# Optimization experiments

Hardware: AMD Instinct MI355X
Metric: run time of the kernel (lower is better)

The kernel has to match this reference:

```python
import jax, jax.numpy as jnp
import numpy as np

N_HEADS = 8  # head_dim = 640 / 8 = 80


def _split_heads(x):
    # [B, S, D] -> [B, H, S, D/H]
    B, S, D = x.shape
    return x.reshape(B, S, N_HEADS, D // N_HEADS).transpose(0, 2, 1, 3)


def _merge_heads(x):
    # [B, H, S, d] -> [B, S, H*d]
    B, H, S, d = x.shape
    return x.transpose(0, 2, 1, 3).reshape(B, S, H * d)


def setup_inputs() -> dict:
    key = jax.random.key(0)
    ks = jax.random.split(key, 12)
    B, S, D, C, A = 4, 2048, 640, 768, 16

    def w(k, fan_in, fan_out, s=1.0):
        return (jax.random.normal(k, (fan_in, fan_out), jnp.float32) / np.sqrt(fan_in) * s)

    return {
        "hidden_states": jax.random.normal(ks[0], (B, S, D), jnp.float32),
        "au_embedding": jax.random.normal(ks[1], (B, A, C), jnp.float32),
        "w_q": w(ks[2], D, D),
        "w_k": w(ks[3], D, D),
        "w_v": w(ks[4], D, D),
        "w_ak": w(ks[5], C, D),
        "w_av": w(ks[6], C, D),
        "w_g1": w(ks[7], D, D // 2),
        "b_g1": jnp.zeros((D // 2,), jnp.float32),
        "w_g2": w(ks[8], D // 2, D, s=0.02),  # near-zero per nn.init.zeros_
        "b_g2": jnp.full((D,), -1.5, jnp.float32),  # per nn.init.constant_(-1.5)
        "w_out": w(ks[9], D, D),
        "b_out": jnp.zeros((D,), jnp.float32),
        "temperature": jnp.full((1,), 5.0, jnp.float32),
    }


def reference(hidden_states, au_embedding, w_q, w_k, w_v, w_ak, w_av,
              w_g1, b_g1, w_g2, b_g2, w_out, b_out, temperature):
    au_scale = 1.0
    residual = hidden_states

    q = _split_heads(hidden_states @ w_q)  # [B,H,S,d]
    k = _split_heads(hidden_states @ w_k)
    v = _split_heads(hidden_states @ w_v)
    d = q.shape[-1]
    scale = 1.0 / jnp.sqrt(jnp.asarray(d, q.dtype))  # attn.scale = head_dim**-0.5

    # main self-attention: QK^T * scale -> softmax -> PV
    probs = jax.nn.softmax(jnp.einsum('bhqd,bhkd->bhqk', q, k) * scale, axis=-1)
    hs = _merge_heads(jnp.einsum('bhqk,bhkd->bhqd', probs, v))  # [B,S,D]

    # AU cross-attention with temperature-scaled logits
    au_k = _split_heads(au_embedding @ w_ak)  # [B,H,A,d]
    au_v = _split_heads(au_embedding @ w_av)
    scaled_alpha = scale * temperature[0]
    au_probs = jax.nn.softmax(jnp.einsum('bhqd,bhkd->bhqk', q, au_k) * scaled_alpha, axis=-1)
    au_hs = _merge_heads(jnp.einsum('bhqk,bhkd->bhqd', au_probs, au_v))  # [B,S,D]

    # gated MLP fusion: sigmoid(Linear(SiLU(Linear(au_hs))))
    gate = jax.nn.sigmoid(jax.nn.silu(au_hs @ w_g1 + b_g1) @ w_g2 + b_g2)
    hs = hs + au_scale * (gate * au_hs)

    hs = hs @ w_out + b_out  # to_out[0]; to_out[1] dropout is identity in eval
    return hs + residual  # residual_connection=True, rescale_output_factor=1.0
```

## Files before the change

### kernel.cpp

```cpp
#include <hip/hip_runtime.h>
#include <stdint.h>

typedef __attribute__((ext_vector_type(8))) short short8;
typedef __attribute__((ext_vector_type(4))) short short4v;
typedef __attribute__((ext_vector_type(4))) float f32x4;

#define DEV static __device__ __forceinline__

DEV short f2bf(float f) {
  union { float f; uint32_t u; } v; v.f = f;
  uint32_t r = (v.u + 0x7fffu + ((v.u >> 16) & 1u)) >> 16;
  return (short)(uint16_t)r;
}
DEV float bf2f(short s) {
  union { uint32_t u; float f; } v; v.u = ((uint32_t)(uint16_t)s) << 16;
  return v.f;
}
DEV int imin(int a, int b) { return a < b ? a : b; }
DEV int xcd_swz(int bid, int nwg) {
  int q8 = nwg >> 3, r8 = nwg & 7;
  int xcd = bid & 7, lin = bid >> 3;
  return (xcd < r8 ? xcd * (q8 + 1) : r8 * (q8 + 1) + (xcd - r8) * q8) + lin;
}


__global__ void k_detect(const uint32_t* __restrict__ src, int* __restrict__ flag) {
  __shared__ int cnt;
  if (threadIdx.x == 0) cnt = 0;
  __syncthreads();
  uint32_t u = src[threadIdx.x];
  int e = (int)((u >> 7) & 0xffu);
  if (e >= 110 && e <= 135) atomicAdd(&cnt, 1);
  __syncthreads();
  if (threadIdx.x == 0) *flag = (cnt > 128) ? 1 : 0;
}

__global__ void k_conv_vec(const void* __restrict__ s1, short* __restrict__ d1, int n1,
                           const void* __restrict__ s2, short* __restrict__ d2, int n2,
                           const int* __restrict__ flag) {
  int i = blockIdx.x * 256 + threadIdx.x;
  const void* src; short* dst;
  if (i < n1) { src = s1; dst = d1; }
  else if (i < n1 + n2) { src = s2; dst = d2; i -= n1; }
  else return;
  if (*flag) {
    ((short4v*)dst)[i] = ((const short4v*)src)[i];
  } else {
    f32x4 v = ((const f32x4*)src)[i];
    short4v o;
    o[0] = f2bf(v[0]); o[1] = f2bf(v[1]); o[2] = f2bf(v[2]); o[3] = f2bf(v[3]);
    ((short4v*)dst)[i] = o;
  }
}

struct WDesc { const void* src; short* dst; int K, N, dstride, tile0; };
struct WTable { WDesc d[8]; };

__global__ void k_conv_w(WTable tb, const int* __restrict__ flag) {
  __shared__ float tile[32][33];
  int tid = blockIdx.x;
  int idx = 0;
#pragma unroll
  for (int i = 1; i < 8; i++) if (tid >= tb.d[i].tile0) idx = i;
  WDesc wd = tb.d[idx];
  int local = tid - wd.tile0;
  int ntiles = wd.N >> 5;
  int n0 = (local % ntiles) * 32, k0 = (local / ntiles) * 32;
  int tx = threadIdx.x, ty = threadIdx.y;
  int isbf = *flag;
#pragma unroll
  for (int i = 0; i < 4; i++) {
    int r = k0 + ty + i * 8, c = n0 + tx;
    float v = 0.f;
    if (r < wd.K && c < wd.N)
      v = isbf ? bf2f(((const short*)wd.src)[(size_t)r * wd.N + c])
               : ((const float*)wd.src)[(size_t)r * wd.N + c];
    tile[ty + i * 8][tx] = v;
  }
  __syncthreads();
#pragma unroll
  for (int i = 0; i < 4; i++) {
    int n = n0 + ty + i * 8, k = k0 + tx;
    if (n < wd.N && k < wd.K) wd.dst[(size_t)n * wd.dstride + k] = f2bf(tile[tx][ty + i * 8]);
  }
}

__global__ void k_conv_bias(const void* b1, const void* b2, const void* b3, const void* tp,
                            float* B1, float* B2, float* B3, float* T,
                            const int* __restrict__ flag) {
  int i = blockIdx.x * 256 + threadIdx.x;
  int isbf = *flag;
  const void* s; float* d; int j;
  if (i < 320) { s = b1; d = B1; j = i; }
  else if (i < 960) { s = b2; d = B2; j = i - 320; }
  else if (i < 1600) { s = b3; d = B3; j = i - 960; }
  else if (i == 1600) { s = tp; d = T; j = 0; }
  else return;
  d[j] = isbf ? bf2f(((const short*)s)[j]) : ((const float*)s)[j];
}

template <int EPI>
__global__ __launch_bounds__(256) void k_gemm_bt(
    const short* __restrict__ A, const short* __restrict__ Wt, void* __restrict__ Cout,
    int M, int N, int K, int nbx,
    const float* __restrict__ bias, const short* __restrict__ x1,
    const short* __restrict__ x2, const short* __restrict__ res) {
  __shared__ __align__(16) short As[128 * 64];
  __shared__ __align__(16) short Bs[128 * 64];
  const int t = threadIdx.x;
  const int w = t >> 6, ln = t & 63;
  const int wm = w >> 1, wn = w & 1;
  const int swz = xcd_swz(blockIdx.x, gridDim.x);
  const int m0 = (swz / nbx) * 128, n0 = (swz % nbx) * 128;
  const int lrow = ln & 15, lg = ln >> 4;

  f32x4 acc[4][4];
#pragma unroll
  for (int i = 0; i < 4; i++)
#pragma unroll
    for (int j = 0; j < 4; j++) acc[i][j] = (f32x4){0.f, 0.f, 0.f, 0.f};

  for (int k0 = 0; k0 < K; k0 += 64) {
    __syncthreads();
#pragma unroll
    for (int c = 0; c < 4; c++) {
      int cc = c * 256 + t;
      int r = cc >> 3, col = (cc & 7) * 8;
      int ra = imin(m0 + r, M - 1);
      int rb = imin(n0 + r, N - 1);
      __builtin_amdgcn_global_load_lds(
          (const __attribute__((address_space(1))) void*)(A + (size_t)ra * K + k0 + col),
          (__attribute__((address_space(3))) void*)&As[(c * 256 + w * 64) * 8],
          16, 0, 0);
      __builtin_amdgcn_global_load_lds(
          (const __attribute__((address_space(1))) void*)(Wt + (size_t)rb * K + k0 + col),
          (__attribute__((address_space(3))) void*)&Bs[(c * 256 + w * 64) * 8],
          16, 0, 0);
    }
    __syncthreads();
    short8 af[4][2], bfr[4][2];
#pragma unroll
    for (int i = 0; i < 4; i++)
#pragma unroll
      for (int kk = 0; kk < 2; kk++) {
        af[i][kk] = *(const short8*)&As[(wm * 64 + i * 16 + lrow) * 64 + lg * 8 + kk * 32];
        bfr[i][kk] = *(const short8*)&Bs[(wn * 64 + i * 16 + lrow) * 64 + lg * 8 + kk * 32];
      }
    __builtin_amdgcn_s_setprio(1);
#pragma unroll
    for (int kk = 0; kk < 2; kk++)
#pragma unroll
      for (int i = 0; i < 4; i++)
#pragma unroll
        for (int j = 0; j < 4; j++)
          acc[i][j] = __builtin_amdgcn_mfma_f32_16x16x32_bf16(af[i][kk], bfr[j][kk], acc[i][j], 0, 0, 0);
    __builtin_amdgcn_s_setprio(0);
  }

  const int rb0 = m0 + wm * 64 + lg * 4;
#pragma unroll
  for (int i = 0; i < 4; i++) {
#pragma unroll
    for (int j = 0; j < 4; j++) {
      int col = n0 + wn * 64 + j * 16 + lrow;
      if (col >= N) continue;
#pragma unroll
      for (int r = 0; r < 4; r++) {
        int row = rb0 + i * 16 + r;
        if (row >= M) continue;
        float v = acc[i][j][r];
        size_t off = (size_t)row * N + col;
        if (EPI == 0) {
          ((short*)Cout)[off] = f2bf(v);
        } else if (EPI == 1) {
          float x = v + bias[col];
          ((short*)Cout)[off] = f2bf(x / (1.f + __expf(-x)));
        } else if (EPI == 2) {
          float g = 1.f / (1.f + __expf(-(v + bias[col])));
          ((short*)Cout)[off] = f2bf(bf2f(x1[off]) + g * bf2f(x2[off]));
        } else {
          ((float*)Cout)[off] = v + bias[col] + bf2f(res[off]);
        }
      }
    }
  }
}

__global__ __launch_bounds__(256) void k_build_vt(const short* __restrict__ qkv,
                                                  short* __restrict__ vt) {
  __shared__ __align__(16) short T[128 * 80];
  const int bh = blockIdx.y, st = blockIdx.x;
  const int b = bh >> 3, h = bh & 7;
  const int t = threadIdx.x;
  for (int c = t; c < 1280; c += 256) {
    int r = c / 10, blk = c % 10;
    *(short8*)&T[r * 80 + blk * 8] =
        *(const short8*)(qkv + (size_t)(b * 2048 + st * 128 + r) * 1920 + 1280 + h * 80 + blk * 8);
  }
  __syncthreads();
  for (int c = t; c < 1280; c += 256) {
    int dd = c % 80, qc = (c / 80) * 8;
    short8 v;
#pragma unroll
    for (int i = 0; i < 8; i++) {
      int q = qc + i;
      int tile = q >> 6, p = q & 63;
      int src = (tile << 6) + (p >> 2) + ((p & 3) << 4);
      v[i] = T[src * 80 + dd];
    }
    *(short8*)(vt + ((size_t)bh * 80 + dd) * 2048 + st * 128 + qc) = v;
  }
}

__global__ __launch_bounds__(512) void k_attn(const short* __restrict__ qkv,
                                              const short* __restrict__ vt,
                                              short* __restrict__ outp) {
  __shared__ __align__(16) short Ks[64 * 104];
  __shared__ __align__(16) char Vs[80 * 128];
  __shared__ __align__(16) char Ps[8][2048];

  const int swzb = xcd_swz(blockIdx.x, 512);
  const int qt = swzb & 15, bh = swzb >> 4;
  const int b = bh >> 3, h = bh & 7;
  const int t = threadIdx.x, w = t >> 6, ln = t & 63;
  const int lg = ln >> 4, lr = ln & 15;
  const float sc2 = 0.111803398875f * 1.4426950408889634f;
  const float SHIFT2 = 32.0f;

  short8 qfrag[3];
  {
    const short* qrow = qkv + (size_t)(b * 2048 + qt * 128 + w * 16 + lr) * 1920 + h * 80;
#pragma unroll
    for (int ks = 0; ks < 3; ks++) {
      int off = ks * 32 + lg * 8;
      short8 v = {0, 0, 0, 0, 0, 0, 0, 0};
      if (off < 80) v = *(const short8*)(qrow + off);
      qfrag[ks] = v;
    }
  }

  const short* kbase = qkv + (size_t)b * 2048 * 1920 + 640 + h * 80;
  const short* vbase = vt + (size_t)bh * 80 * 2048;

  int kr0 = t / 12, kb0 = t % 12;
  int kr1 = (t + 512) / 12, kb1 = (t + 512) % 12;
  int vr0 = t >> 3, vb0 = t & 7;
  int vr1 = (t + 512) >> 3, vb1 = (t + 512) & 7;
  const bool kv1 = (t < 256), vv1 = (t < 128);

  short8 kreg0 = {0,0,0,0,0,0,0,0}, kreg1 = kreg0, vreg0 = kreg0, vreg1 = kreg0;

  if (kb0 < 10) kreg0 = *(const short8*)(kbase + (size_t)kr0 * 1920 + kb0 * 8);
  if (kv1 && kb1 < 10) kreg1 = *(const short8*)(kbase + (size_t)kr1 * 1920 + kb1 * 8);
  vreg0 = *(const short8*)(vbase + (size_t)vr0 * 2048 + vb0 * 8);
  if (vv1) vreg1 = *(const short8*)(vbase + (size_t)vr1 * 2048 + vb1 * 8);

  f32x4 oacc[5];
#pragma unroll
  for (int f = 0; f < 5; f++) oacc[f] = (f32x4){0.f, 0.f, 0.f, 0.f};
  float psacc[4] = {0.f, 0.f, 0.f, 0.f};

  for (int kt = 0; kt < 32; kt++) {
    __syncthreads();
    *(short8*)&Ks[kr0 * 104 + kb0 * 8] = kreg0;
    if (kv1) *(short8*)&Ks[kr1 * 104 + kb1 * 8] = kreg1;
    {
      int dst0 = (vr0 * 128 + vb0 * 16) ^ ((vr0 & 7) << 4);
      *(short8*)&Vs[dst0] = vreg0;
      if (vv1) {
        int dst1 = (vr1 * 128 + vb1 * 16) ^ ((vr1 & 7) << 4);
        *(short8*)&Vs[dst1] = vreg1;
      }
    }
    __syncthreads();

    if (kt < 31) {
      const short* kb2 = kbase + (size_t)(kt + 1) * 64 * 1920;
      const short* vb2 = vbase + (size_t)(kt + 1) * 64;
      if (kb0 < 10) kreg0 = *(const short8*)(kb2 + (size_t)kr0 * 1920 + kb0 * 8);
      if (kv1 && kb1 < 10) kreg1 = *(const short8*)(kb2 + (size_t)kr1 * 1920 + kb1 * 8);
      vreg0 = *(const short8*)(vb2 + (size_t)vr0 * 2048 + vb0 * 8);
      if (vv1) vreg1 = *(const short8*)(vb2 + (size_t)vr1 * 2048 + vb1 * 8);
    }

    f32x4 sf[4];
#pragma unroll
    for (int j = 0; j < 4; j++) sf[j] = (f32x4){0.f, 0.f, 0.f, 0.f};
    __builtin_amdgcn_s_setprio(1);
#pragma unroll
    for (int ks = 0; ks < 3; ks++) {
#pragma unroll
      for (int j = 0; j < 4; j++) {
        short8 bk = *(const short8*)&Ks[(j * 16 + lr) * 104 + ks * 32 + lg * 8];
        sf[j] = __builtin_amdgcn_mfma_f32_16x16x32_bf16(qfrag[ks], bk, sf[j], 0, 0, 0);
      }
    }
    __builtin_amdgcn_s_setprio(0);

    char* Pw = Ps[w];
#pragma unroll
    for (int r = 0; r < 4; r++) {
      int row = lg * 4 + r;
      float p0 = exp2f(sf[0][r] * sc2 - SHIFT2);
      float p1 = exp2f(sf[1][r] * sc2 - SHIFT2);
      float p2 = exp2f(sf[2][r] * sc2 - SHIFT2);
      float p3 = exp2f(sf[3][r] * sc2 - SHIFT2);
      psacc[r] += (p0 + p1) + (p2 + p3);
      short4v pk;
      pk[0] = f2bf(p0); pk[1] = f2bf(p1); pk[2] = f2bf(p2); pk[3] = f2bf(p3);
      int addr = (row * 128 + lr * 8) ^ ((row & 7) << 4);
      *(short4v*)&Pw[addr] = pk;
    }

    __builtin_amdgcn_s_setprio(1);
#pragma unroll
    for (int ks = 0; ks < 2; ks++) {
      short8 ap = *(const short8*)&Pw[(lr * 128 + ks * 64 + lg * 16) ^ ((lr & 7) << 4)];
#pragma unroll
      for (int f = 0; f < 5; f++) {
        int vrow = f * 16 + lr;
        short8 bv = *(const short8*)&Vs[(vrow * 128 + ks * 64 + lg * 16) ^ ((vrow & 7) << 4)];
        oacc[f] = __builtin_amdgcn_mfma_f32_16x16x32_bf16(ap, bv, oacc[f], 0, 0, 0);
      }
    }
    __builtin_amdgcn_s_setprio(0);
  }

  float lrowv[4];
#pragma unroll
  for (int r = 0; r < 4; r++) {
    float sum = psacc[r];
#pragma unroll
    for (int off = 8; off >= 1; off >>= 1) sum += __shfl_xor(sum, off, 64);
    lrowv[r] = sum;
  }

#pragma unroll
  for (int f = 0; f < 5; f++) {
#pragma unroll
    for (int r = 0; r < 4; r++) {
      int q = qt * 128 + w * 16 + lg * 4 + r;
      float o = oacc[f][r] / lrowv[r];
      outp[(size_t)(b * 2048 + q) * 640 + h * 80 + f * 16 + lr] = f2bf(o);
    }
  }
}

__global__ __launch_bounds__(256) void k_au_attn(const short* __restrict__ qkv,
                                                 const short* __restrict__ aukv,
                                                 const float* __restrict__ temp,
                                                 short* __restrict__ auhs) {
  __shared__ __align__(16) short aK[16 * 640];
  __shared__ __align__(16) short aV[16 * 640];
  const int b = blockIdx.y;
  const int t = threadIdx.x;
  for (int c = t; c < 2560; c += 256) {
    int arr = c / 1280, cc = c - arr * 1280;
    int r = cc / 80, blk = cc % 80;
    const short* s = aukv + (size_t)(b * 16 + r) * 1280 + arr * 640 + blk * 8;
    short* d = (arr ? aV : aK) + r * 640 + blk * 8;
    *(short8*)d = *(const short8*)s;
  }
  __syncthreads();
  const int sl = t & 31, h = t >> 5;
  const int s = blockIdx.x * 32 + sl;
  const float alpha = 0.111803398875f * temp[0];
  const float LOG2E = 1.4426950408889634f;

  float qf[80];
  {
    const short* q = qkv + (size_t)(b * 2048 + s) * 1920 + h * 80;
#pragma unroll
    for (int c = 0; c < 10; c++) {
      short8 v = *(const short8*)(q + c * 8);
#pragma unroll
      for (int j = 0; j < 8; j++) qf[c * 8 + j] = bf2f(v[j]);
    }
  }
  float lgt[16];
#pragma unroll
  for (int a = 0; a < 16; a++) {
    const short* kr = &aK[a * 640 + h * 80];
    float acc = 0.f;
#pragma unroll
    for (int c = 0; c < 10; c++) {
      short8 v = *(const short8*)(kr + c * 8);
#pragma unroll
      for (int j = 0; j < 8; j++) acc += qf[c * 8 + j] * bf2f(v[j]);
    }
    lgt[a] = acc * alpha;
  }
  float m = lgt[0];
#pragma unroll
  for (int a = 1; a < 16; a++) m = fmaxf(m, lgt[a]);
  float se = 0.f;
#pragma unroll
  for (int a = 0; a < 16; a++) { lgt[a] = exp2f((lgt[a] - m) * LOG2E); se += lgt[a]; }
  float inv = 1.f / se;

  float o[80];
#pragma unroll
  for (int i = 0; i < 80; i++) o[i] = 0.f;
#pragma unroll
  for (int a = 0; a < 16; a++) {
    float pa = lgt[a] * inv;
    const short* vr = &aV[a * 640 + h * 80];
#pragma unroll
    for (int c = 0; c < 10; c++) {
      short8 v = *(const short8*)(vr + c * 8);
#pragma unroll
      for (int j = 0; j < 8; j++) o[c * 8 + j] += pa * bf2f(v[j]);
    }
  }
  short* op = auhs + (size_t)(b * 2048 + s) * 640 + h * 80;
#pragma unroll
  for (int c = 0; c < 10; c++) {
    short8 v;
#pragma unroll
    for (int j = 0; j < 8; j++) v[j] = f2bf(o[c * 8 + j]);
    *(short8*)(op + c * 8) = v;
  }
}

extern "C" void kernel_launch(void* const* d_in, const int* in_sizes, int n_in,
                              void* d_out, int out_size, void* d_ws, size_t ws_size,
                              hipStream_t stream) {
  (void)in_sizes; (void)n_in; (void)out_size; (void)ws_size;

  const void* hidden = d_in[0];
  const void* auemb  = d_in[1];

  char* ws = (char*)d_ws;
  int* FLAG   = (int*)(ws + 0);
  float* BG1  = (float*)(ws + 1024);
  float* BG2  = (float*)(ws + 4096);
  float* BOUT = (float*)(ws + 8192);
  float* TEMP = (float*)(ws + 12288);

  size_t o = 16384;
  short* HSB = (short*)(ws + o);    o += 10485760;
  short* AUB = (short*)(ws + o);    o += 98304;
  short* WQKVT = (short*)(ws + o);  o += 2457600;
  short* WAKVT = (short*)(ws + o);  o += 1966080;
  short* WG1T = (short*)(ws + o);   o += 409600;
  short* WG2T = (short*)(ws + o);   o += 409600;
  short* WOUTT = (short*)(ws + o);  o += 819200;
  short* QKV = (short*)(ws + o);    o += 31457280;
  short* VT = (short*)(ws + o);     o += 10485760;
  short* AUKV = (short*)(ws + o);   o += 163840;
  short* HSATTN = (short*)(ws + o); o += 10485760;
  short* AUHS = (short*)(ws + o);   o += 10485760;
  short* G1 = QKV;
  short* HSMIX = QKV + 5242880;

  k_detect<<<1, 256, 0, stream>>>((const uint32_t*)hidden, FLAG);

  k_conv_vec<<<5168, 256, 0, stream>>>(hidden, HSB, 1310720, auemb, AUB, 12288, FLAG);

  WTable tb;
  tb.d[0] = { d_in[2],  WQKVT,              640, 640, 640, 0    };
  tb.d[1] = { d_in[3],  WQKVT + 409600,     640, 640, 640, 400  };
  tb.d[2] = { d_in[4],  WQKVT + 819200,     640, 640, 640, 800  };
  tb.d[3] = { d_in[5],  WAKVT,              768, 640, 768, 1200 };
  tb.d[4] = { d_in[6],  WAKVT + 640 * 768,  768, 640, 768, 1680 };
  tb.d[5] = { d_in[7],  WG1T,               640, 320, 640, 2160 };
  tb.d[6] = { d_in[9],  WG2T,               320, 640, 320, 2360 };
  tb.d[7] = { d_in[11], WOUTT,              640, 640, 640, 2560 };
  k_conv_w<<<2960, dim3(32, 8), 0, stream>>>(tb, FLAG);
  k_conv_bias<<<7, 256, 0, stream>>>(d_in[8], d_in[10], d_in[12], d_in[13],
                                     BG1, BG2, BOUT, TEMP, FLAG);

  k_gemm_bt<0><<<960, 256, 0, stream>>>(HSB, WQKVT, QKV, 8192, 1920, 640, 15,
                                        nullptr, nullptr, nullptr, nullptr);
  k_gemm_bt<0><<<10, 256, 0, stream>>>(AUB, WAKVT, AUKV, 64, 1280, 768, 10,
                                       nullptr, nullptr, nullptr, nullptr);

  k_build_vt<<<dim3(16, 32), 256, 0, stream>>>(QKV, VT);
  k_attn<<<512, 512, 0, stream>>>(QKV, VT, HSATTN);
  k_au_attn<<<dim3(64, 4), 256, 0, stream>>>(QKV, AUKV, TEMP, AUHS);

  k_gemm_bt<1><<<192, 256, 0, stream>>>(AUHS, WG1T, G1, 8192, 320, 640, 3,
                                        BG1, nullptr, nullptr, nullptr);
  k_gemm_bt<2><<<320, 256, 0, stream>>>(G1, WG2T, HSMIX, 8192, 640, 320, 5,
                                        BG2, HSATTN, AUHS, nullptr);
  k_gemm_bt<3><<<320, 256, 0, stream>>>(HSMIX, WOUTT, d_out, 8192, 640, 640, 5,
                                        BOUT, nullptr, nullptr, HSB);
}
```

Measured before the change: 344.6 us.

## Merge prep, projection, and AU-attention launches into fewer fused kernels

```diff
diff --git a/kernel.cpp b/kernel.cpp
--- a/kernel.cpp
+++ b/kernel.cpp
@@ -4,6 +4,7 @@
 typedef __attribute__((ext_vector_type(8))) short short8;
 typedef __attribute__((ext_vector_type(4))) short short4v;
 typedef __attribute__((ext_vector_type(4))) float f32x4;
+typedef __attribute__((ext_vector_type(2))) uint32_t u32x2;
 
 #define DEV static __device__ __forceinline__
 
@@ -16,102 +17,98 @@
   union { uint32_t u; float f; } v; v.u = ((uint32_t)(uint16_t)s) << 16;
   return v.f;
 }
+DEV uint32_t fbits(float f) { union { float f; uint32_t u; } v; v.f = f; return v.u; }
 DEV int imin(int a, int b) { return a < b ? a : b; }
 DEV int xcd_swz(int bid, int nwg) {
   int q8 = nwg >> 3, r8 = nwg & 7;
   int xcd = bid & 7, lin = bid >> 3;
   return (xcd < r8 ? xcd * (q8 + 1) : r8 * (q8 + 1) + (xcd - r8) * q8) + lin;
 }
-
-
-__global__ void k_detect(const uint32_t* __restrict__ src, int* __restrict__ flag) {
+DEV int detect_flag(const uint32_t* src, int t) {
   __shared__ int cnt;
-  if (threadIdx.x == 0) cnt = 0;
+  if (t == 0) cnt = 0;
   __syncthreads();
-  uint32_t u = src[threadIdx.x];
+  uint32_t u = src[t & 255];
   int e = (int)((u >> 7) & 0xffu);
   if (e >= 110 && e <= 135) atomicAdd(&cnt, 1);
   __syncthreads();
-  if (threadIdx.x == 0) *flag = (cnt > 128) ? 1 : 0;
-}
-
-__global__ void k_conv_vec(const void* __restrict__ s1, short* __restrict__ d1, int n1,
-                           const void* __restrict__ s2, short* __restrict__ d2, int n2,
-                           const int* __restrict__ flag) {
-  int i = blockIdx.x * 256 + threadIdx.x;
-  const void* src; short* dst;
-  if (i < n1) { src = s1; dst = d1; }
-  else if (i < n1 + n2) { src = s2; dst = d2; i -= n1; }
-  else return;
-  if (*flag) {
-    ((short4v*)dst)[i] = ((const short4v*)src)[i];
-  } else {
-    f32x4 v = ((const f32x4*)src)[i];
-    short4v o;
-    o[0] = f2bf(v[0]); o[1] = f2bf(v[1]); o[2] = f2bf(v[2]); o[3] = f2bf(v[3]);
-    ((short4v*)dst)[i] = o;
-  }
-}
+  return cnt > 128;
+}
+
 
 struct WDesc { const void* src; short* dst; int K, N, dstride, tile0; };
 struct WTable { WDesc d[8]; };
 
-__global__ void k_conv_w(WTable tb, const int* __restrict__ flag) {
-  __shared__ float tile[32][33];
-  int tid = blockIdx.x;
-  int idx = 0;
-#pragma unroll
-  for (int i = 1; i < 8; i++) if (tid >= tb.d[i].tile0) idx = i;
-  WDesc wd = tb.d[idx];
-  int local = tid - wd.tile0;
-  int ntiles = wd.N >> 5;
-  int n0 = (local % ntiles) * 32, k0 = (local / ntiles) * 32;
-  int tx = threadIdx.x, ty = threadIdx.y;
-  int isbf = *flag;
-#pragma unroll
-  for (int i = 0; i < 4; i++) {
-    int r = k0 + ty + i * 8, c = n0 + tx;
-    float v = 0.f;
-    if (r < wd.K && c < wd.N)
-      v = isbf ? bf2f(((const short*)wd.src)[(size_t)r * wd.N + c])
-               : ((const float*)wd.src)[(size_t)r * wd.N + c];
-    tile[ty + i * 8][tx] = v;
-  }
-  __syncthreads();
-#pragma unroll
-  for (int i = 0; i < 4; i++) {
-    int n = n0 + ty + i * 8, k = k0 + tx;
-    if (n < wd.N && k < wd.K) wd.dst[(size_t)n * wd.dstride + k] = f2bf(tile[tx][ty + i * 8]);
-  }
-}
-
-__global__ void k_conv_bias(const void* b1, const void* b2, const void* b3, const void* tp,
-                            float* B1, float* B2, float* B3, float* T,
-                            const int* __restrict__ flag) {
-  int i = blockIdx.x * 256 + threadIdx.x;
-  int isbf = *flag;
-  const void* s; float* d; int j;
-  if (i < 320) { s = b1; d = B1; j = i; }
-  else if (i < 960) { s = b2; d = B2; j = i - 320; }
-  else if (i < 1600) { s = b3; d = B3; j = i - 960; }
-  else if (i == 1600) { s = tp; d = T; j = 0; }
-  else return;
-  d[j] = isbf ? bf2f(((const short*)s)[j]) : ((const float*)s)[j];
+__global__ __launch_bounds__(256) void k_prep(
+    const void* __restrict__ hidden, const void* __restrict__ auemb,
+    short* __restrict__ HSB, short* __restrict__ AUB, WTable tb,
+    const void* b1, const void* b2, const void* b3, const void* tp,
+    float* B1, float* B2, float* B3, float* T) {
+  const int t = threadIdx.x;
+  const int isbf = detect_flag((const uint32_t*)hidden, t);
+  const int bid = blockIdx.x;
+
+  if (bid < 5168) {
+    int i = bid * 256 + t;
+    const void* src; short* dst;
+    if (i < 1310720) { src = hidden; dst = HSB; }
+    else { src = auemb; dst = AUB; i -= 1310720; }
+    if (isbf) {
+      ((short4v*)dst)[i] = ((const short4v*)src)[i];
+    } else {
+      f32x4 v = ((const f32x4*)src)[i];
+      short4v o;
+      o[0] = f2bf(v[0]); o[1] = f2bf(v[1]); o[2] = f2bf(v[2]); o[3] = f2bf(v[3]);
+      ((short4v*)dst)[i] = o;
+    }
+  } else if (bid < 8128) {
+    __shared__ float tile[32][33];
+    int tid = bid - 5168;
+    int idx = 0;
+#pragma unroll
+    for (int i = 1; i < 8; i++) if (tid >= tb.d[i].tile0) idx = i;
+    WDesc wd = tb.d[idx];
+    int local = tid - wd.tile0;
+    int ntiles = wd.N >> 5;
+    int n0 = (local % ntiles) * 32, k0 = (local / ntiles) * 32;
+    int tx = t & 31, ty = t >> 5;
+#pragma unroll
+    for (int i = 0; i < 4; i++) {
+      int r = k0 + ty + i * 8, c = n0 + tx;
+      float v = 0.f;
+      if (r < wd.K && c < wd.N)
+        v = isbf ? bf2f(((const short*)wd.src)[(size_t)r * wd.N + c])
+                 : ((const float*)wd.src)[(size_t)r * wd.N + c];
+      tile[ty + i * 8][tx] = v;
+    }
+    __syncthreads();
+#pragma unroll
+    for (int i = 0; i < 4; i++) {
+      int n = n0 + ty + i * 8, k = k0 + tx;
+      if (n < wd.N && k < wd.K) wd.dst[(size_t)n * wd.dstride + k] = f2bf(tile[tx][ty + i * 8]);
+    }
+  } else {
+    int i = (bid - 8128) * 256 + t;
+    const void* s; float* d; int j;
+    if (i < 320) { s = b1; d = B1; j = i; }
+    else if (i < 960) { s = b2; d = B2; j = i - 320; }
+    else if (i < 1600) { s = b3; d = B3; j = i - 960; }
+    else if (i == 1600) { s = tp; d = T; j = 0; }
+    else return;
+    d[j] = isbf ? bf2f(((const short*)s)[j]) : ((const float*)s)[j];
+  }
 }
 
 template <int EPI>
-__global__ __launch_bounds__(256) void k_gemm_bt(
-    const short* __restrict__ A, const short* __restrict__ Wt, void* __restrict__ Cout,
-    int M, int N, int K, int nbx,
-    const float* __restrict__ bias, const short* __restrict__ x1,
-    const short* __restrict__ x2, const short* __restrict__ res) {
+DEV void gemm_core(const short* __restrict__ A, const short* __restrict__ Wt,
+                   void* __restrict__ Cout, int M, int N, int K, int m0, int n0,
+                   const float* __restrict__ bias, const short* __restrict__ x1,
+                   const short* __restrict__ x2, const short* __restrict__ res) {
   __shared__ __align__(16) short As[128 * 64];
   __shared__ __align__(16) short Bs[128 * 64];
   const int t = threadIdx.x;
   const int w = t >> 6, ln = t & 63;
   const int wm = w >> 1, wn = w & 1;
-  const int swz = xcd_swz(blockIdx.x, gridDim.x);
-  const int m0 = (swz / nbx) * 128, n0 = (swz % nbx) * 128;
   const int lrow = ln & 15, lg = ln >> 4;
 
   f32x4 acc[4][4];
@@ -186,29 +183,134 @@
   }
 }
 
-__global__ __launch_bounds__(256) void k_build_vt(const short* __restrict__ qkv,
-                                                  short* __restrict__ vt) {
-  __shared__ __align__(16) short T[128 * 80];
-  const int bh = blockIdx.y, st = blockIdx.x;
-  const int b = bh >> 3, h = bh & 7;
+template <int EPI>
+__global__ __launch_bounds__(256) void k_gemm_bt(
+    const short* __restrict__ A, const short* __restrict__ Wt, void* __restrict__ Cout,
+    int M, int N, int K, int nbx,
+    const float* __restrict__ bias, const short* __restrict__ x1,
+    const short* __restrict__ x2, const short* __restrict__ res) {
+  const int swz = xcd_swz(blockIdx.x, gridDim.x);
+  gemm_core<EPI>(A, Wt, Cout, M, N, K, (swz / nbx) * 128, (swz % nbx) * 128,
+                 bias, x1, x2, res);
+}
+
+__global__ __launch_bounds__(256) void k_gemm_fused(
+    const short* __restrict__ A0, const short* __restrict__ W0, short* __restrict__ C0,
+    const short* __restrict__ A1, const short* __restrict__ W1, short* __restrict__ C1) {
+  const int bid = blockIdx.x;
+  if (bid < 960) {
+    int swz = xcd_swz(bid, 960);
+    gemm_core<0>(A0, W0, C0, 8192, 1920, 640, (swz / 15) * 128, (swz % 15) * 128,
+                 nullptr, nullptr, nullptr, nullptr);
+  } else {
+    int local = bid - 960;
+    gemm_core<0>(A1, W1, C1, 64, 1280, 768, 0, local * 128,
+                 nullptr, nullptr, nullptr, nullptr);
+  }
+}
+
+__global__ __launch_bounds__(256) void k_vt_au(const short* __restrict__ qkv,
+                                               short* __restrict__ vt,
+                                               const short* __restrict__ aukv,
+                                               const float* __restrict__ temp,
+                                               short* __restrict__ auhs) {
+  __shared__ __align__(16) short SH[20480];
+  const int bid = blockIdx.x;
   const int t = threadIdx.x;
-  for (int c = t; c < 1280; c += 256) {
-    int r = c / 10, blk = c % 10;
-    *(short8*)&T[r * 80 + blk * 8] =
-        *(const short8*)(qkv + (size_t)(b * 2048 + st * 128 + r) * 1920 + 1280 + h * 80 + blk * 8);
-  }
-  __syncthreads();
-  for (int c = t; c < 1280; c += 256) {
-    int dd = c % 80, qc = (c / 80) * 8;
-    short8 v;
-#pragma unroll
-    for (int i = 0; i < 8; i++) {
-      int q = qc + i;
-      int tile = q >> 6, p = q & 63;
-      int src = (tile << 6) + (p >> 2) + ((p & 3) << 4);
-      v[i] = T[src * 80 + dd];
-    }
-    *(short8*)(vt + ((size_t)bh * 80 + dd) * 2048 + st * 128 + qc) = v;
+
+  if (bid < 512) {
+    short* T = SH;
+    const int st = bid & 15, bh = bid >> 4;
+    const int b = bh >> 3, h = bh & 7;
+    for (int c = t; c < 1280; c += 256) {
+      int r = c / 10, blk = c % 10;
+      *(short8*)&T[r * 80 + blk * 8] =
+          *(const short8*)(qkv + (size_t)(b * 2048 + st * 128 + r) * 1920 + 1280 + h * 80 + blk * 8);
+    }
+    __syncthreads();
+    for (int c = t; c < 1280; c += 256) {
+      int dd = c % 80, qc = (c / 80) * 8;
+      short8 v;
+#pragma unroll
+      for (int i = 0; i < 8; i++) {
+        int q = qc + i;
+        int tile = q >> 6, p = q & 63;
+        int src = (tile << 6) + (p >> 2) + ((p & 3) << 4);
+        v[i] = T[src * 80 + dd];
+      }
+      *(short8*)(vt + ((size_t)bh * 80 + dd) * 2048 + st * 128 + qc) = v;
+    }
+  } else {
+    short* aK = SH;
+    short* aV = SH + 16 * 640;
+    const int bid2 = bid - 512;
+    const int sx = bid2 & 63, b = bid2 >> 6;
+    for (int c = t; c < 2560; c += 256) {
+      int arr = c / 1280, cc = c - arr * 1280;
+      int r = cc / 80, blk = cc % 80;
+      const short* s = aukv + (size_t)(b * 16 + r) * 1280 + arr * 640 + blk * 8;
+      short* d = (arr ? aV : aK) + r * 640 + blk * 8;
+      *(short8*)d = *(const short8*)s;
+    }
+    __syncthreads();
+    const int sl = t & 31, h = t >> 5;
+    const int s = sx * 32 + sl;
+    const float alpha = 0.111803398875f * temp[0];
+    const float LOG2E = 1.4426950408889634f;
+
+    float qf[80];
+    {
+      const short* q = qkv + (size_t)(b * 2048 + s) * 1920 + h * 80;
+#pragma unroll
+      for (int c = 0; c < 10; c++) {
+        short8 v = *(const short8*)(q + c * 8);
+#pragma unroll
+        for (int j = 0; j < 8; j++) qf[c * 8 + j] = bf2f(v[j]);
+      }
+    }
+    float lgt[16];
+#pragma unroll
+    for (int a = 0; a < 16; a++) {
+      const short* kr = &aK[a * 640 + h * 80];
+      float acc = 0.f;
+#pragma unroll
+      for (int c = 0; c < 10; c++) {
+        short8 v = *(const short8*)(kr + c * 8);
+#pragma unroll
+        for (int j = 0; j < 8; j++) acc += qf[c * 8 + j] * bf2f(v[j]);
+      }
+      lgt[a] = acc * alpha;
+    }
+    float m = lgt[0];
+#pragma unroll
+    for (int a = 1; a < 16; a++) m = fmaxf(m, lgt[a]);
+    float se = 0.f;
+#pragma unroll
+    for (int a = 0; a < 16; a++) { lgt[a] = exp2f((lgt[a] - m) * LOG2E); se += lgt[a]; }
+    float inv = 1.f / se;
+
+    float o[80];
+#pragma unroll
+    for (int i = 0; i < 80; i++) o[i] = 0.f;
+#pragma unroll
+    for (int a = 0; a < 16; a++) {
+      float pa = lgt[a] * inv;
+      const short* vr = &aV[a * 640 + h * 80];
+#pragma unroll
+      for (int c = 0; c < 10; c++) {
+        short8 v = *(const short8*)(vr + c * 8);
+#pragma unroll
+        for (int j = 0; j < 8; j++) o[c * 8 + j] += pa * bf2f(v[j]);
+      }
+    }
+    short* op = auhs + (size_t)(b * 2048 + s) * 640 + h * 80;
+#pragma unroll
+    for (int c = 0; c < 10; c++) {
+      short8 v;
+#pragma unroll
+      for (int j = 0; j < 8; j++) v[j] = f2bf(o[c * 8 + j]);
+      *(short8*)(op + c * 8) = v;
+    }
   }
 }
 
@@ -306,10 +408,11 @@
       float p2 = exp2f(sf[2][r] * sc2 - SHIFT2);
       float p3 = exp2f(sf[3][r] * sc2 - SHIFT2);
       psacc[r] += (p0 + p1) + (p2 + p3);
-      short4v pk;
-      pk[0] = f2bf(p0); pk[1] = f2bf(p1); pk[2] = f2bf(p2); pk[3] = f2bf(p3);
+      u32x2 pk;
+      pk[0] = (fbits(p0) >> 16) | (fbits(p1) & 0xffff0000u);
+      pk[1] = (fbits(p2) >> 16) | (fbits(p3) & 0xffff0000u);
       int addr = (row * 128 + lr * 8) ^ ((row & 7) << 4);
-      *(short4v*)&Pw[addr] = pk;
+      *(u32x2*)&Pw[addr] = pk;
     }
 
     __builtin_amdgcn_s_setprio(1);
@@ -346,82 +449,6 @@
   }
 }
 
-__global__ __launch_bounds__(256) void k_au_attn(const short* __restrict__ qkv,
-                                                 const short* __restrict__ aukv,
-                                                 const float* __restrict__ temp,
-                                                 short* __restrict__ auhs) {
-  __shared__ __align__(16) short aK[16 * 640];
-  __shared__ __align__(16) short aV[16 * 640];
-  const int b = blockIdx.y;
-  const int t = threadIdx.x;
-  for (int c = t; c < 2560; c += 256) {
-    int arr = c / 1280, cc = c - arr * 1280;
-    int r = cc / 80, blk = cc % 80;
-    const short* s = aukv + (size_t)(b * 16 + r) * 1280 + arr * 640 + blk * 8;
-    short* d = (arr ? aV : aK) + r * 640 + blk * 8;
-    *(short8*)d = *(const short8*)s;
-  }
-  __syncthreads();
-  const int sl = t & 31, h = t >> 5;
-  const int s = blockIdx.x * 32 + sl;
-  const float alpha = 0.111803398875f * temp[0];
-  const float LOG2E = 1.4426950408889634f;
-
-  float qf[80];
-  {
-    const short* q = qkv + (size_t)(b * 2048 + s) * 1920 + h * 80;
-#pragma unroll
-    for (int c = 0; c < 10; c++) {
-      short8 v = *(const short8*)(q + c * 8);
-#pragma unroll
-      for (int j = 0; j < 8; j++) qf[c * 8 + j] = bf2f(v[j]);
-    }
-  }
-  float lgt[16];
-#pragma unroll
-  for (int a = 0; a < 16; a++) {
-    const short* kr = &aK[a * 640 + h * 80];
-    float acc = 0.f;
-#pragma unroll
-    for (int c = 0; c < 10; c++) {
-      short8 v = *(const short8*)(kr + c * 8);
-#pragma unroll
-      for (int j = 0; j < 8; j++) acc += qf[c * 8 + j] * bf2f(v[j]);
-    }
-    lgt[a] = acc * alpha;
-  }
-  float m = lgt[0];
-#pragma unroll
-  for (int a = 1; a < 16; a++) m = fmaxf(m, lgt[a]);
-  float se = 0.f;
-#pragma unroll
-  for (int a = 0; a < 16; a++) { lgt[a] = exp2f((lgt[a] - m) * LOG2E); se += lgt[a]; }
-  float inv = 1.f / se;
-
-  float o[80];
-#pragma unroll
-  for (int i = 0; i < 80; i++) o[i] = 0.f;
-#pragma unroll
-  for (int a = 0; a < 16; a++) {
-    float pa = lgt[a] * inv;
-    const short* vr = &aV[a * 640 + h * 80];
-#pragma unroll
-    for (int c = 0; c < 10; c++) {
-      short8 v = *(const short8*)(vr + c * 8);
-#pragma unroll
-      for (int j = 0; j < 8; j++) o[c * 8 + j] += pa * bf2f(v[j]);
-    }
-  }
-  short* op = auhs + (size_t)(b * 2048 + s) * 640 + h * 80;
-#pragma unroll
-  for (int c = 0; c < 10; c++) {
-    short8 v;
-#pragma unroll
-    for (int j = 0; j < 8; j++) v[j] = f2bf(o[c * 8 + j]);
-    *(short8*)(op + c * 8) = v;
-  }
-}
-
 extern "C" void kernel_launch(void* const* d_in, const int* in_sizes, int n_in,
                               void* d_out, int out_size, void* d_ws, size_t ws_size,
                               hipStream_t stream) {
@@ -431,7 +458,6 @@
   const void* auemb  = d_in[1];
 
   char* ws = (char*)d_ws;
-  int* FLAG   = (int*)(ws + 0);
   float* BG1  = (float*)(ws + 1024);
   float* BG2  = (float*)(ws + 4096);
   float* BOUT = (float*)(ws + 8192);
@@ -453,10 +479,6 @@
   short* G1 = QKV;
   short* HSMIX = QKV + 5242880;
 
-  k_detect<<<1, 256, 0, stream>>>((const uint32_t*)hidden, FLAG);
-
-  k_conv_vec<<<5168, 256, 0, stream>>>(hidden, HSB, 1310720, auemb, AUB, 12288, FLAG);
-
   WTable tb;
   tb.d[0] = { d_in[2],  WQKVT,              640, 640, 640, 0    };
   tb.d[1] = { d_in[3],  WQKVT + 409600,     640, 640, 640, 400  };
@@ -466,19 +488,13 @@
   tb.d[5] = { d_in[7],  WG1T,               640, 320, 640, 2160 };
   tb.d[6] = { d_in[9],  WG2T,               320, 640, 320, 2360 };
   tb.d[7] = { d_in[11], WOUTT,              640, 640, 640, 2560 };
-  k_conv_w<<<2960, dim3(32, 8), 0, stream>>>(tb, FLAG);
-  k_conv_bias<<<7, 256, 0, stream>>>(d_in[8], d_in[10], d_in[12], d_in[13],
-                                     BG1, BG2, BOUT, TEMP, FLAG);
-
-  k_gemm_bt<0><<<960, 256, 0, stream>>>(HSB, WQKVT, QKV, 8192, 1920, 640, 15,
-                                        nullptr, nullptr, nullptr, nullptr);
-  k_gemm_bt<0><<<10, 256, 0, stream>>>(AUB, WAKVT, AUKV, 64, 1280, 768, 10,
-                                       nullptr, nullptr, nullptr, nullptr);
-
-  k_build_vt<<<dim3(16, 32), 256, 0, stream>>>(QKV, VT);
+
+  k_prep<<<8135, 256, 0, stream>>>(hidden, auemb, HSB, AUB, tb,
+                                   d_in[8], d_in[10], d_in[12], d_in[13],
+                                   BG1, BG2, BOUT, TEMP);
+  k_gemm_fused<<<970, 256, 0, stream>>>(HSB, WQKVT, QKV, AUB, WAKVT, AUKV);
+  k_vt_au<<<768, 256, 0, stream>>>(QKV, VT, AUKV, TEMP, AUHS);
   k_attn<<<512, 512, 0, stream>>>(QKV, VT, HSATTN);
-  k_au_attn<<<dim3(64, 4), 256, 0, stream>>>(QKV, AUKV, TEMP, AUHS);
-
   k_gemm_bt<1><<<192, 256, 0, stream>>>(AUHS, WG1T, G1, 8192, 320, 640, 3,
                                         BG1, nullptr, nullptr, nullptr);
   k_gemm_bt<2><<<320, 256, 0, stream>>>(G1, WG2T, HSMIX, 8192, 640, 320, 5,
```

Result: faster. 308.5 us (-10.5%).
